# Optimization experiments

Measured on AMD Instinct MI355X. Metric: run time of the kernel, lower is better.

Reference implementation:

```python
import jax, jax.numpy as jnp
import numpy as np

NUM_HEADS = 16
NEG_INF = -9000000000000000.0


def setup_inputs() -> dict:
    key = jax.random.key(0)
    ks = jax.random.split(key, 4)
    B, S, D = 2, 2048, 1024
    x = jax.random.normal(ks[0], (B, S, D), dtype=jnp.float32)
    mask = jax.random.randint(ks[1], (1, 1, S, S), 0, 2, dtype=jnp.int32)
    # xavier-uniform-ish init scaled down for stability
    w_qkv = jax.random.normal(ks[2], (3 * D, D), dtype=jnp.float32) * (1.0 / np.sqrt(D))
    b_qkv = jnp.zeros((3 * D,), dtype=jnp.float32)
    w_o = jax.random.normal(ks[3], (D, D), dtype=jnp.float32) * (1.0 / np.sqrt(D))
    b_o = jnp.zeros((D,), dtype=jnp.float32)
    return {"x": x, "mask": mask, "w_qkv": w_qkv, "b_qkv": b_qkv, "w_o": w_o, "b_o": b_o}


def reference(x, mask, w_qkv, b_qkv, w_o, b_o):
    B, S, D = x.shape
    H = NUM_HEADS
    hd = D // H
    # qkv projection: torch Linear is x @ W.T + b
    qkv = x @ w_qkv.T + b_qkv                      # [B, S, 3D]
    qkv = qkv.reshape(B, S, H, 3 * hd).transpose(0, 2, 1, 3)  # [B, H, S, 3hd]
    q, k, v = jnp.split(qkv, 3, axis=-1)           # each [B, H, S, hd]
    scale = 1.0 / np.sqrt(hd).astype(np.float32)
    logits = jnp.einsum("bhqd,bhkd->bhqk", q, k) * scale  # [B, H, S, S]
    logits = jnp.where(mask == 0, NEG_INF, logits)
    attn = jax.nn.softmax(logits, axis=-1)
    ctx = jnp.einsum("bhqk,bhkd->bhqd", attn, v)   # [B, H, S, hd]
    ctx = ctx.transpose(0, 2, 1, 3).reshape(B, S, D)
    return ctx @ w_o.T + b_o
```

## Files before the change

kernel.cpp:

```cpp
#include <hip/hip_runtime.h>

typedef __attribute__((ext_vector_type(8))) short short8;
typedef __attribute__((ext_vector_type(4))) float f32x4;

#define MFMA16(a, b, c) __builtin_amdgcn_mfma_f32_16x16x32_bf16(a, b, c, 0, 0, 0)

#define BATCH 2
#define SEQ 2048
#define DMODEL 1024
#define NHEADS 16
#define HDIM 64
#define MROWS (BATCH * SEQ)
#define N_QKV (3 * DMODEL)

#define QSCALE 0.1803368801111184f

#define GLDS16(gp, lp)                                                       \
  __builtin_amdgcn_global_load_lds(                                          \
      (const __attribute__((address_space(1))) void*)(gp),                   \
      (__attribute__((address_space(3))) void*)(lp), 16, 0, 0)

static __device__ __forceinline__ unsigned short f2bf(float f) {
  unsigned int u = __float_as_uint(f);
  u = (u + 0x7fff + ((u >> 16) & 1)) >> 16;
  return (unsigned short)u;
}

static __device__ __forceinline__ unsigned int pk2bf(float lo, float hi) {
  unsigned int r;
  asm("v_cvt_pk_bf16_f32 %0, %1, %2" : "=v"(r) : "v"(lo), "v"(hi));
  return r;
}

static __device__ __forceinline__ float fexp2(float x) {
  float r;
  asm("v_exp_f32 %0, %1" : "=v"(r) : "v"(x));
  return r;
}

__global__ void cvt3_kernel(const float* __restrict__ a, unsigned short* __restrict__ oa,
                            int na4, const float* __restrict__ b,
                            unsigned short* __restrict__ ob, int nb4,
                            const float* __restrict__ c,
                            unsigned short* __restrict__ oc, int nc4) {
  int i = blockIdx.x * blockDim.x + threadIdx.x;
  const float* src;
  unsigned short* dst;
  int j = i;
  if (j < na4) {
    src = a; dst = oa;
  } else if ((j -= na4) < nb4) {
    src = b; dst = ob;
  } else if ((j -= nb4) < nc4) {
    src = c; dst = oc;
  } else
    return;
  f32x4 v = ((const f32x4*)src)[j];
  ushort4 o;
  o.x = f2bf(v[0]); o.y = f2bf(v[1]); o.z = f2bf(v[2]); o.w = f2bf(v[3]);
  ((ushort4*)dst)[j] = o;
}

__global__ void mask_to_bits(const int* __restrict__ mask,
                             unsigned int* __restrict__ bits) {
  int i = blockIdx.x * blockDim.x + threadIdx.x;
  unsigned long long b = __ballot(mask[i] != 0);
  if ((threadIdx.x & 63) == 0)
    ((unsigned long long*)bits)[i >> 6] = b;
}

template <int EPI>
__global__ __launch_bounds__(256) void gemm_bt(
    const unsigned short* __restrict__ A, const unsigned short* __restrict__ Bm,
    const float* __restrict__ bias, int Kdim, int Ndim,
    unsigned short* __restrict__ qb, unsigned short* __restrict__ kb,
    unsigned short* __restrict__ vtb, float* __restrict__ Cout) {
  __shared__ __align__(16) unsigned short lA[128 * 32];
  __shared__ __align__(16) unsigned short lB[128 * 32];

  int t = threadIdx.x;
  int nwg = gridDim.x * gridDim.y;
  int lin = blockIdx.y * gridDim.x + blockIdx.x;
  int swb = (lin & 7) * (nwg >> 3) + (lin >> 3);
  int m0 = (swb / gridDim.x) * 128, n0 = (swb % gridDim.x) * 128;

  int w = t >> 6, lane = t & 63, quad = lane >> 4, l16 = lane & 15;
  int wm = (w >> 1) * 64, wn = (w & 1) * 64;

  f32x4 acc[4][4];
#pragma unroll
  for (int i = 0; i < 4; ++i)
#pragma unroll
    for (int j = 0; j < 4; ++j) acc[i][j] = (f32x4){0.f, 0.f, 0.f, 0.f};

  int nK = Kdim >> 5;
  for (int kk = 0; kk < nK; ++kk) {
    __syncthreads();
#pragma unroll
    for (int c = 0; c < 2; ++c) {
      int id = t + c * 256;
      GLDS16(&A[(size_t)(m0 + (id >> 2)) * Kdim + (kk << 5) + ((id & 3) << 3)],
             (char*)lA + (id & ~63) * 16);
      GLDS16(&Bm[(size_t)(n0 + (id >> 2)) * Kdim + (kk << 5) + ((id & 3) << 3)],
             (char*)lB + (id & ~63) * 16);
    }
    __syncthreads();
    short8 af[4], bfr[4];
#pragma unroll
    for (int i = 0; i < 4; ++i)
      af[i] = *(const short8*)&lA[(wm + i * 16 + l16) * 32 + quad * 8];
#pragma unroll
    for (int j = 0; j < 4; ++j)
      bfr[j] = *(const short8*)&lB[(wn + j * 16 + l16) * 32 + quad * 8];
#pragma unroll
    for (int i = 0; i < 4; ++i)
#pragma unroll
      for (int j = 0; j < 4; ++j) acc[i][j] = MFMA16(af[i], bfr[j], acc[i][j]);
  }

#pragma unroll
  for (int j = 0; j < 4; ++j) {
    int n = n0 + wn + j * 16 + l16;
    float bs = bias[n];
#pragma unroll
    for (int i = 0; i < 4; ++i) {
#pragma unroll
      for (int r = 0; r < 4; ++r) {
        int m = m0 + wm + i * 16 + quad * 4 + r;
        float v = acc[i][j][r] + bs;
        if (EPI == 0) {
          int b = m >> 11, s = m & 2047;
          int h = n / 192, rr = n % 192;
          int bh = (b << 4) + h;
          if (rr < 64)
            qb[((size_t)bh * SEQ + s) * HDIM + rr] = f2bf(v * QSCALE);
          else if (rr < 128)
            kb[((size_t)bh * SEQ + s) * HDIM + (rr - 64)] = f2bf(v);
          else
            vtb[((size_t)bh * HDIM + (rr - 128)) * SEQ + s] = f2bf(v);
        } else {
          Cout[(size_t)m * Ndim + n] = v;
        }
      }
    }
  }
}

__global__ __launch_bounds__(256, 4) void attn_kernel(
    const unsigned short* __restrict__ qbuf, const unsigned short* __restrict__ kbuf,
    const unsigned short* __restrict__ vtbuf, const unsigned int* __restrict__ mbits,
    unsigned short* __restrict__ ctx) {
  __shared__ __align__(16) unsigned short lK[2][64 * 64];
  __shared__ __align__(16) unsigned short lV[2][64 * 64];
  __shared__ __align__(16) unsigned short lP[64 * 64];

  int lin = blockIdx.y * gridDim.x + blockIdx.x;
  int slin = (lin & 7) * 128 + (lin >> 3);
  int qt = slin & 31, bh = slin >> 5;
  int q0 = qt * 64;
  const unsigned short* Q = qbuf + (size_t)bh * SEQ * HDIM;
  const unsigned short* K = kbuf + (size_t)bh * SEQ * HDIM;
  const unsigned short* VT = vtbuf + (size_t)bh * HDIM * SEQ;

  int t = threadIdx.x;
  int w = t >> 6, lane = t & 63, quad = lane >> 4, l16 = lane & 15;
  int swz = (l16 & 7) << 4;

  int qrow = q0 + w * 16 + l16;
  short8 qf0 = *(const short8*)&Q[(size_t)qrow * HDIM + quad * 8];
  short8 qf1 = *(const short8*)&Q[(size_t)qrow * HDIM + 32 + quad * 8];

  const short one = (short)0x3F80;
  short8 ones = {one, one, one, one, one, one, one, one};

  f32x4 o[4];
#pragma unroll
  for (int jt = 0; jt < 4; ++jt) o[jt] = (f32x4){0.f, 0.f, 0.f, 0.f};
  f32x4 li4 = (f32x4){0.f, 0.f, 0.f, 0.f};
  float mi = 0.f;

  int scol = ((lane & 7) ^ (lane >> 3)) << 3;
  const unsigned short* gK = K + (size_t)(w * 8 + (lane >> 3)) * HDIM + scol;
  const unsigned short* gV = VT + (size_t)(w * 8 + (lane >> 3)) * SEQ + scol;

#define STAGE_KV(buf)                                            \
  do {                                                           \
    GLDS16(gK, &lK[buf][(w * 8) * 64]);                          \
    GLDS16(gK + 32 * HDIM, &lK[buf][(32 + w * 8) * 64]);         \
    GLDS16(gV, &lV[buf][(w * 8) * 64]);                          \
    GLDS16(gV + 32 * SEQ, &lV[buf][(32 + w * 8) * 64]);          \
  } while (0)

  STAGE_KV(0);
  gK += 64 * HDIM;
  gV += 64;

  const unsigned int* mrow = mbits + (size_t)qrow * 64;
  unsigned short* lPr = &lP[(w * 16 + l16) * 64];

  for (int it = 0; it < SEQ / 64; ++it) {
    __syncthreads();
    if (it + 1 < SEQ / 64) {
      STAGE_KV((it + 1) & 1);
      gK += 64 * HDIM;
      gV += 64;
    }
    const unsigned short* cK = lK[it & 1];
    const unsigned short* cV = lV[it & 1];

    uint2 mw = *(const uint2*)&mrow[it * 2];

    f32x4 s[4];
    __builtin_amdgcn_s_setprio(1);
#pragma unroll
    for (int j = 0; j < 4; ++j) {
      const char* kr = (const char*)&cK[(j * 16 + l16) * 64];
      short8 ka = *(const short8*)(kr + ((quad * 16) ^ swz));
      short8 kc = *(const short8*)(kr + ((64 + quad * 16) ^ swz));
      f32x4 z = (f32x4){0.f, 0.f, 0.f, 0.f};
      z = MFMA16(ka, qf0, z);
      z = MFMA16(kc, qf1, z);
      s[j] = z;
    }
    __builtin_amdgcn_s_setprio(0);

    unsigned int ma = mw.x >> (quad * 4);
    unsigned int mb = mw.y >> (quad * 4);
#pragma unroll
    for (int j = 0; j < 4; ++j) {
      unsigned int sel = (j < 2) ? ma : mb;
      int sh = (j & 1) << 4;
#pragma unroll
      for (int r = 0; r < 4; ++r)
        s[j][r] = (sel & (1u << (sh + r))) ? s[j][r] : -1e30f;
    }

    float a0 = fmaxf(fmaxf(s[0][0], s[0][1]), s[0][2]);
    float a1 = fmaxf(fmaxf(s[0][3], s[1][0]), s[1][1]);
    float a2 = fmaxf(fmaxf(s[1][2], s[1][3]), s[2][0]);
    float a3 = fmaxf(fmaxf(s[2][1], s[2][2]), s[2][3]);
    float a4 = fmaxf(fmaxf(s[3][0], s[3][1]), s[3][2]);
    float b0 = fmaxf(fmaxf(a0, a1), a2);
    float b1 = fmaxf(fmaxf(a3, a4), s[3][3]);
    float mx = fmaxf(b0, b1);
    mx = fmaxf(mx, __shfl_xor(mx, 16));
    mx = fmaxf(mx, __shfl_xor(mx, 32));

#pragma unroll
    for (int j = 0; j < 4; ++j)
#pragma unroll
      for (int r = 0; r < 4; ++r) s[j][r] = fexp2(s[j][r] - mi);

    if (!__all(mx <= mi + 5.f)) {
      float mn = fmaxf(mi, mx);
      float al = fexp2(mi - mn);
#pragma unroll
      for (int j = 0; j < 4; ++j)
#pragma unroll
        for (int r = 0; r < 4; ++r) s[j][r] *= al;
#pragma unroll
      for (int jt = 0; jt < 4; ++jt)
#pragma unroll
        for (int r = 0; r < 4; ++r) o[jt][r] *= al;
#pragma unroll
      for (int r = 0; r < 4; ++r) li4[r] *= al;
      mi = mn;
    }

#pragma unroll
    for (int j = 0; j < 4; ++j) {
      uint2 u;
      u.x = pk2bf(s[j][0], s[j][1]);
      u.y = pk2bf(s[j][2], s[j][3]);
      *(uint2*)((char*)lPr + ((j * 32 + quad * 8) ^ swz)) = u;
    }

    __builtin_amdgcn_s_setprio(1);
#pragma unroll
    for (int kh = 0; kh < 2; ++kh) {
      short8 pf = *(const short8*)((const char*)lPr + ((kh * 64 + quad * 16) ^ swz));
      li4 = MFMA16(ones, pf, li4);
#pragma unroll
      for (int jt = 0; jt < 4; ++jt) {
        const char* vr = (const char*)&cV[(jt * 16 + l16) * 64];
        short8 vf = *(const short8*)(vr + ((kh * 64 + quad * 16) ^ swz));
        o[jt] = MFMA16(vf, pf, o[jt]);
      }
    }
    __builtin_amdgcn_s_setprio(0);
  }

  float inv = 1.0f / li4[0];
  int b = bh >> 4, h = bh & 15;
  unsigned short* crow = ctx + ((size_t)(b * SEQ + qrow)) * DMODEL + h * HDIM;
#pragma unroll
  for (int jt = 0; jt < 4; ++jt) {
    uint2 u;
    u.x = pk2bf(o[jt][0] * inv, o[jt][1] * inv);
    u.y = pk2bf(o[jt][2] * inv, o[jt][3] * inv);
    *(uint2*)&crow[jt * 16 + quad * 4] = u;
  }
}

extern "C" void kernel_launch(void* const* d_in, const int* in_sizes, int n_in,
                              void* d_out, int out_size, void* d_ws, size_t ws_size,
                              hipStream_t stream) {
  const float* x = (const float*)d_in[0];
  const int* mask = (const int*)d_in[1];
  const float* w_qkv = (const float*)d_in[2];
  const float* b_qkv = (const float*)d_in[3];
  const float* w_o = (const float*)d_in[4];
  const float* b_o = (const float*)d_in[5];
  float* out = (float*)d_out;

  char* ws = (char*)d_ws;
  unsigned short* xb = (unsigned short*)(ws);
  unsigned short* wqkvb = (unsigned short*)(ws + (8ull << 20));
  unsigned short* wob = (unsigned short*)(ws + (14ull << 20));
  unsigned short* qb = (unsigned short*)(ws + (16ull << 20));
  unsigned short* kb = (unsigned short*)(ws + (24ull << 20));
  unsigned short* vtb = (unsigned short*)(ws + (32ull << 20));
  unsigned short* ctx = (unsigned short*)(ws + (40ull << 20));
  unsigned int* mbits = (unsigned int*)(ws + (48ull << 20));

  const int na4 = (MROWS * DMODEL) / 4;
  const int nb4 = (N_QKV * DMODEL) / 4;
  const int nc4 = (DMODEL * DMODEL) / 4;
  cvt3_kernel<<<(na4 + nb4 + nc4 + 255) / 256, 256, 0, stream>>>(
      x, xb, na4, w_qkv, wqkvb, nb4, w_o, wob, nc4);
  mask_to_bits<<<(SEQ * SEQ) / 256, 256, 0, stream>>>(mask, mbits);

  gemm_bt<0><<<dim3(N_QKV / 128, MROWS / 128), 256, 0, stream>>>(
      xb, wqkvb, b_qkv, DMODEL, N_QKV, qb, kb, vtb, nullptr);

  attn_kernel<<<dim3(SEQ / 64, BATCH * NHEADS), 256, 0, stream>>>(
      qb, kb, vtb, mbits, ctx);

  gemm_bt<1><<<dim3(DMODEL / 128, MROWS / 128), 256, 0, stream>>>(
      ctx, wob, b_o, DMODEL, DMODEL, nullptr, nullptr, nullptr, out);
}
```

Baseline: 234.2 us.

## Double-buffer GEMM LDS with swizzle, merge prep kernels, defer softmax max reduce

After: 224.5 us. 4.2% less time.

```diff
diff --git a/kernel.cpp b/kernel.cpp
--- a/kernel.cpp
+++ b/kernel.cpp
@@ -20,6 +20,8 @@
       (const __attribute__((address_space(1))) void*)(gp),                   \
       (__attribute__((address_space(3))) void*)(lp), 16, 0, 0)
 
+#define CFENCE() asm volatile("" ::: "memory")
+
 static __device__ __forceinline__ unsigned short f2bf(float f) {
   unsigned int u = __float_as_uint(f);
   u = (u + 0x7fff + ((u >> 16) & 1)) >> 16;
@@ -38,15 +40,23 @@
   return r;
 }
 
-__global__ void cvt3_kernel(const float* __restrict__ a, unsigned short* __restrict__ oa,
+__global__ void prep_kernel(const int* __restrict__ mask,
+                            unsigned int* __restrict__ bits,
+                            const float* __restrict__ a, unsigned short* __restrict__ oa,
                             int na4, const float* __restrict__ b,
                             unsigned short* __restrict__ ob, int nb4,
                             const float* __restrict__ c,
                             unsigned short* __restrict__ oc, int nc4) {
-  int i = blockIdx.x * blockDim.x + threadIdx.x;
+  if (blockIdx.x < (SEQ * SEQ) / 256) {
+    int i = blockIdx.x * 256 + threadIdx.x;
+    unsigned long long bl = __ballot(mask[i] != 0);
+    if ((threadIdx.x & 63) == 0)
+      ((unsigned long long*)bits)[i >> 6] = bl;
+    return;
+  }
+  int j = (blockIdx.x - (SEQ * SEQ) / 256) * 256 + threadIdx.x;
   const float* src;
   unsigned short* dst;
-  int j = i;
   if (j < na4) {
     src = a; dst = oa;
   } else if ((j -= na4) < nb4) {
@@ -61,22 +71,14 @@
   ((ushort4*)dst)[j] = o;
 }
 
-__global__ void mask_to_bits(const int* __restrict__ mask,
-                             unsigned int* __restrict__ bits) {
-  int i = blockIdx.x * blockDim.x + threadIdx.x;
-  unsigned long long b = __ballot(mask[i] != 0);
-  if ((threadIdx.x & 63) == 0)
-    ((unsigned long long*)bits)[i >> 6] = b;
-}
-
 template <int EPI>
-__global__ __launch_bounds__(256) void gemm_bt(
+__global__ __launch_bounds__(256, 4) void gemm_bt(
     const unsigned short* __restrict__ A, const unsigned short* __restrict__ Bm,
     const float* __restrict__ bias, int Kdim, int Ndim,
     unsigned short* __restrict__ qb, unsigned short* __restrict__ kb,
     unsigned short* __restrict__ vtb, float* __restrict__ Cout) {
-  __shared__ __align__(16) unsigned short lA[128 * 32];
-  __shared__ __align__(16) unsigned short lB[128 * 32];
+  __shared__ __align__(16) unsigned short lA[2][128 * 32];
+  __shared__ __align__(16) unsigned short lB[2][128 * 32];
 
   int t = threadIdx.x;
   int nwg = gridDim.x * gridDim.y;
@@ -94,28 +96,51 @@
     for (int j = 0; j < 4; ++j) acc[i][j] = (f32x4){0.f, 0.f, 0.f, 0.f};
 
   int nK = Kdim >> 5;
+
+#define GSTAGE(buf, kk)                                                      \
+  do {                                                                       \
+    for (int c = 0; c < 2; ++c) {                                            \
+      int id = t + c * 256;                                                  \
+      int row = id >> 2;                                                     \
+      int gc = ((id & 3) ^ (row & 3)) << 3; \
+      GLDS16(&A[(size_t)(m0 + row) * Kdim + ((kk) << 5) + gc],               \
+             (char*)lA[buf] + (id & ~63) * 16);                              \
+      GLDS16(&Bm[(size_t)(n0 + row) * Kdim + ((kk) << 5) + gc],              \
+             (char*)lB[buf] + (id & ~63) * 16);                              \
+    }                                                                        \
+  } while (0)
+
+  GSTAGE(0, 0);
   for (int kk = 0; kk < nK; ++kk) {
-    __syncthreads();
-#pragma unroll
-    for (int c = 0; c < 2; ++c) {
-      int id = t + c * 256;
-      GLDS16(&A[(size_t)(m0 + (id >> 2)) * Kdim + (kk << 5) + ((id & 3) << 3)],
-             (char*)lA + (id & ~63) * 16);
-      GLDS16(&Bm[(size_t)(n0 + (id >> 2)) * Kdim + (kk << 5) + ((id & 3) << 3)],
-             (char*)lB + (id & ~63) * 16);
-    }
-    __syncthreads();
+    int cur = kk & 1;
+    if (kk + 1 < nK) {
+      GSTAGE(cur ^ 1, kk + 1);
+      asm volatile("s_waitcnt vmcnt(4)" ::: "memory");
+    } else {
+      asm volatile("s_waitcnt vmcnt(0)" ::: "memory");
+    }
+    __builtin_amdgcn_s_barrier();
+    CFENCE();
+    __builtin_amdgcn_sched_barrier(0);
+
     short8 af[4], bfr[4];
+    int rswz = (l16 & 3) << 4;
 #pragma unroll
     for (int i = 0; i < 4; ++i)
-      af[i] = *(const short8*)&lA[(wm + i * 16 + l16) * 32 + quad * 8];
+      af[i] = *(const short8*)((const char*)&lA[cur][(wm + i * 16 + l16) * 32] +
+                               ((quad * 16) ^ rswz));
 #pragma unroll
     for (int j = 0; j < 4; ++j)
-      bfr[j] = *(const short8*)&lB[(wn + j * 16 + l16) * 32 + quad * 8];
+      bfr[j] = *(const short8*)((const char*)&lB[cur][(wn + j * 16 + l16) * 32] +
+                                ((quad * 16) ^ rswz));
 #pragma unroll
     for (int i = 0; i < 4; ++i)
 #pragma unroll
       for (int j = 0; j < 4; ++j) acc[i][j] = MFMA16(af[i], bfr[j], acc[i][j]);
+
+    asm volatile("s_waitcnt lgkmcnt(0)" ::: "memory");
+    __builtin_amdgcn_s_barrier();
+    CFENCE();
   }
 
 #pragma unroll
@@ -243,8 +268,6 @@
     float b0 = fmaxf(fmaxf(a0, a1), a2);
     float b1 = fmaxf(fmaxf(a3, a4), s[3][3]);
     float mx = fmaxf(b0, b1);
-    mx = fmaxf(mx, __shfl_xor(mx, 16));
-    mx = fmaxf(mx, __shfl_xor(mx, 32));
 
 #pragma unroll
     for (int j = 0; j < 4; ++j)
@@ -252,6 +275,8 @@
       for (int r = 0; r < 4; ++r) s[j][r] = fexp2(s[j][r] - mi);
 
     if (!__all(mx <= mi + 5.f)) {
+      mx = fmaxf(mx, __shfl_xor(mx, 16));
+      mx = fmaxf(mx, __shfl_xor(mx, 32));
       float mn = fmaxf(mi, mx);
       float al = fexp2(mi - mn);
 #pragma unroll
@@ -326,9 +351,10 @@
   const int na4 = (MROWS * DMODEL) / 4;
   const int nb4 = (N_QKV * DMODEL) / 4;
   const int nc4 = (DMODEL * DMODEL) / 4;
-  cvt3_kernel<<<(na4 + nb4 + nc4 + 255) / 256, 256, 0, stream>>>(
-      x, xb, na4, w_qkv, wqkvb, nb4, w_o, wob, nc4);
-  mask_to_bits<<<(SEQ * SEQ) / 256, 256, 0, stream>>>(mask, mbits);
+  const int nmask = (SEQ * SEQ) / 256;
+  const int ncvt = (na4 + nb4 + nc4 + 255) / 256;
+  prep_kernel<<<nmask + ncvt, 256, 0, stream>>>(mask, mbits, x, xb, na4,
+                                                w_qkv, wqkvb, nb4, w_o, wob, nc4);
 
   gemm_bt<0><<<dim3(N_QKV / 128, MROWS / 128), 256, 0, stream>>>(
       xb, wqkvb, b_qkv, DMODEL, N_QKV, qb, kb, vtb, nullptr);
```
